# Performance work log

Hardware: AMD Instinct MI355X
Metric: run time of the kernel (lower is better)

The kernel has to match this reference:

```python
import jax, jax.numpy as jnp
import numpy as np
import math

B, S, D, H, DFF = 4, 1024, 1024, 16, 4096
DK = D // H
EPS = 1e-5


def setup_inputs() -> dict:
    key = jax.random.key(0)
    ks = jax.random.split(key, 16)
    sc = 0.02
    inp = {
        "x": jax.random.normal(ks[0], (B, S, D), jnp.float32),
        "Wq": jax.random.normal(ks[1], (D, D), jnp.float32) * sc,
        "bq": jnp.zeros((D,), jnp.float32),
        "Wk": jax.random.normal(ks[2], (D, D), jnp.float32) * sc,
        "bk": jnp.zeros((D,), jnp.float32),
        "Wv": jax.random.normal(ks[3], (D, D), jnp.float32) * sc,
        "bv": jnp.zeros((D,), jnp.float32),
        "Wo": jax.random.normal(ks[4], (D, D), jnp.float32) * sc,
        "bo": jnp.zeros((D,), jnp.float32),
        "W1": jax.random.normal(ks[5], (D, DFF), jnp.float32) * sc,
        "b1": jnp.zeros((DFF,), jnp.float32),
        "W2": jax.random.normal(ks[6], (DFF, D), jnp.float32) * sc,
        "b2": jnp.zeros((D,), jnp.float32),
        "g1": jnp.ones((D,), jnp.float32),
        "be1": jnp.zeros((D,), jnp.float32),
        "g2": jnp.ones((D,), jnp.float32),
        "be2": jnp.zeros((D,), jnp.float32),
    }
    return inp


def _layernorm(x, g, b):
    mu = jnp.mean(x, axis=-1, keepdims=True)
    var = jnp.mean(jnp.square(x - mu), axis=-1, keepdims=True)
    return (x - mu) * jax.lax.rsqrt(var + EPS) * g + b


def reference(x, Wq, bq, Wk, bk, Wv, bv, Wo, bo, W1, b1, W2, b2, g1, be1, g2, be2):
    # multi-head self-attention (dropout = identity, eval mode)
    q = (x @ Wq + bq).reshape(B, S, H, DK).transpose(0, 2, 1, 3)  # [B,H,S,DK]
    k = (x @ Wk + bk).reshape(B, S, H, DK).transpose(0, 2, 1, 3)
    v = (x @ Wv + bv).reshape(B, S, H, DK).transpose(0, 2, 1, 3)
    scores = jnp.einsum("bhqd,bhkd->bhqk", q, k) / math.sqrt(DK)
    attn_weights = jax.nn.softmax(scores, axis=-1)
    ctx = jnp.einsum("bhqk,bhkd->bhqd", attn_weights, v)
    ctx = ctx.transpose(0, 2, 1, 3).reshape(B, S, D)
    attn_out = ctx @ Wo + bo
    x = _layernorm(x + attn_out, g1, be1)
    ff = jax.nn.relu(x @ W1 + b1) @ W2 + b2
    x = _layernorm(x + ff, g2, be2)
    return x, attn_weights
```

## Files before the change

### kernel.cpp

```cpp
#include <hip/hip_runtime.h>

typedef unsigned short u16;
typedef __attribute__((ext_vector_type(8))) short bf16x8;
typedef __attribute__((ext_vector_type(8))) unsigned short u16x8;
typedef __attribute__((ext_vector_type(4))) float f32x4;

__device__ __forceinline__ u16 f2b(float f) {
  unsigned u = __float_as_uint(f);
  u += 0x7fffu + ((u >> 16) & 1u);
  return (u16)(u >> 16);
}

__global__ __launch_bounds__(256) void cast_k(const float* __restrict__ s,
                                              u16* __restrict__ d, int n4) {
  int i = blockIdx.x * 256 + threadIdx.x;
  if (i >= n4) return;
  float4 v = *(const float4*)(s + (size_t)i * 4);
  ushort4 o = make_ushort4(f2b(v.x), f2b(v.y), f2b(v.z), f2b(v.w));
  *(ushort4*)(d + (size_t)i * 4) = o;
}

__global__ __launch_bounds__(256) void transpose_k(const float* __restrict__ src,
                                                   u16* __restrict__ dst,
                                                   int ldsrc, int lddst) {
  __shared__ float t[32][33];
  int c0 = blockIdx.x * 32, r0 = blockIdx.y * 32;
  int tx = threadIdx.x, ty = threadIdx.y;
#pragma unroll
  for (int i = 0; i < 4; ++i)
    t[ty + i * 8][tx] = src[(size_t)(r0 + ty + i * 8) * ldsrc + c0 + tx];
  __syncthreads();
#pragma unroll
  for (int i = 0; i < 4; ++i)
    dst[(size_t)(c0 + ty + i * 8) * lddst + r0 + tx] = f2b(t[tx][ty + i * 8]);
}

__global__ __launch_bounds__(256) void transpose_v_k(const u16* __restrict__ qkv,
                                                     u16* __restrict__ vt) {
  __shared__ u16 t[32][33];
  int z = blockIdx.z;
  int b = z >> 4, h = z & 15;
  int s0 = blockIdx.x * 32, d0 = blockIdx.y * 32;
  int tx = threadIdx.x, ty = threadIdx.y;
  const u16* src = qkv + (size_t)(b * 1024) * 3072 + 2048 + h * 64;
  u16* dst = vt + (size_t)z * 65536;
#pragma unroll
  for (int i = 0; i < 4; ++i)
    t[ty + i * 8][tx] = src[(size_t)(s0 + ty + i * 8) * 3072 + d0 + tx];
  __syncthreads();
#pragma unroll
  for (int i = 0; i < 4; ++i)
    dst[(size_t)(d0 + ty + i * 8) * 1024 + s0 + tx] = t[tx][ty + i * 8];
}

template <int BN, int AF32, int BIAS, int RELU, int SB16, int SF32>
__global__ __launch_bounds__(256) void gemm_k(
    const u16* __restrict__ Ab, const float* __restrict__ Af,
    long aHi, long aLo, int lda,
    const u16* __restrict__ Bt, long bHi, long bLo, int ldb,
    float* __restrict__ Cf, u16* __restrict__ Cb,
    long cHi, long cLo, int ldc,
    const float* __restrict__ bias, int K, int ZD) {
  constexpr int NT = BN / 32;
  __shared__ u16 As[128 * 40];
  __shared__ u16 Bs[BN * 40];

  const int tid = threadIdx.x;
  const int lane = tid & 63;
  const int wave = tid >> 6;
  const int waveM = wave >> 1, waveN = wave & 1;
  const int quad = lane >> 4, l16 = lane & 15;

  const int zb = blockIdx.z / ZD, zr = blockIdx.z % ZD;
  const long aOff = zb * aHi + zr * aLo;
  const long bOff = zb * bHi + zr * bLo;
  const long cOff = zb * cHi + zr * cLo;

  const int row0 = blockIdx.y * 128;
  const int col0 = blockIdx.x * BN;

  f32x4 acc[4][NT] = {};

  for (int k0 = 0; k0 < K; k0 += 32) {
#pragma unroll
    for (int it = 0; it < 2; ++it) {
      int e = (it * 256 + tid) * 8;
      int r = e >> 5, c = e & 31;
      if (AF32) {
        const float4* p = (const float4*)(Af + aOff + (long)(row0 + r) * lda + k0 + c);
        float4 v0 = p[0], v1 = p[1];
        u16x8 wv;
        wv[0] = f2b(v0.x); wv[1] = f2b(v0.y); wv[2] = f2b(v0.z); wv[3] = f2b(v0.w);
        wv[4] = f2b(v1.x); wv[5] = f2b(v1.y); wv[6] = f2b(v1.z); wv[7] = f2b(v1.w);
        *(u16x8*)&As[r * 40 + c] = wv;
      } else {
        uint4 v = *(const uint4*)(Ab + aOff + (long)(row0 + r) * lda + k0 + c);
        *(uint4*)&As[r * 40 + c] = v;
      }
    }
#pragma unroll
    for (int it = 0; it < BN / 64; ++it) {
      int e = (it * 256 + tid) * 8;
      int r = e >> 5, c = e & 31;
      uint4 v = *(const uint4*)(Bt + bOff + (long)(col0 + r) * ldb + k0 + c);
      *(uint4*)&Bs[r * 40 + c] = v;
    }
    __syncthreads();

    bf16x8 af[4], bfr[NT];
#pragma unroll
    for (int mi = 0; mi < 4; ++mi)
      af[mi] = *(const bf16x8*)&As[(waveM * 64 + mi * 16 + l16) * 40 + quad * 8];
#pragma unroll
    for (int ni = 0; ni < NT; ++ni)
      bfr[ni] = *(const bf16x8*)&Bs[(waveN * (BN / 2) + ni * 16 + l16) * 40 + quad * 8];
#pragma unroll
    for (int mi = 0; mi < 4; ++mi)
#pragma unroll
      for (int ni = 0; ni < NT; ++ni)
        acc[mi][ni] = __builtin_amdgcn_mfma_f32_16x16x32_bf16(af[mi], bfr[ni], acc[mi][ni], 0, 0, 0);
    __syncthreads();
  }

#pragma unroll
  for (int ni = 0; ni < NT; ++ni) {
    int col = col0 + waveN * (BN / 2) + ni * 16 + l16;
    float bv = BIAS ? bias[col] : 0.f;
#pragma unroll
    for (int mi = 0; mi < 4; ++mi) {
#pragma unroll
      for (int r = 0; r < 4; ++r) {
        int row = row0 + waveM * 64 + mi * 16 + quad * 4 + r;
        float v = acc[mi][ni][r] + bv;
        if (RELU) v = fmaxf(v, 0.f);
        long idx = cOff + (long)row * ldc + col;
        if (SF32) Cf[idx] = v;
        if (SB16) Cb[idx] = f2b(v);
      }
    }
  }
}

__global__ __launch_bounds__(256) void softmax_k(float* __restrict__ a) {
  long row = blockIdx.x;
  int tid = threadIdx.x;
  float* p = a + row * 1024 + tid * 4;
  float4 v = *(const float4*)p;
  float m = fmaxf(fmaxf(v.x, v.y), fmaxf(v.z, v.w));
#pragma unroll
  for (int d = 32; d > 0; d >>= 1) m = fmaxf(m, __shfl_xor(m, d));
  __shared__ float red[4];
  if ((tid & 63) == 0) red[tid >> 6] = m;
  __syncthreads();
  m = fmaxf(fmaxf(red[0], red[1]), fmaxf(red[2], red[3]));
  v.x = __expf((v.x - m) * 0.125f);
  v.y = __expf((v.y - m) * 0.125f);
  v.z = __expf((v.z - m) * 0.125f);
  v.w = __expf((v.w - m) * 0.125f);
  float s = v.x + v.y + v.z + v.w;
#pragma unroll
  for (int d = 32; d > 0; d >>= 1) s += __shfl_xor(s, d);
  __shared__ float red2[4];
  if ((tid & 63) == 0) red2[tid >> 6] = s;
  __syncthreads();
  s = red2[0] + red2[1] + red2[2] + red2[3];
  float r = 1.f / s;
  v.x *= r; v.y *= r; v.z *= r; v.w *= r;
  *(float4*)p = v;
}

template <int WB16>
__global__ __launch_bounds__(256) void add_ln_k(const float* __restrict__ xp,
                                                const float* __restrict__ yp,
                                                const float* __restrict__ g,
                                                const float* __restrict__ bta,
                                                float* __restrict__ of,
                                                u16* __restrict__ ob) {
  long row = blockIdx.x;
  int tid = threadIdx.x;
  const float4 xv = *(const float4*)(xp + row * 1024 + tid * 4);
  const float4 yv = *(const float4*)(yp + row * 1024 + tid * 4);
  float4 v = make_float4(xv.x + yv.x, xv.y + yv.y, xv.z + yv.z, xv.w + yv.w);
  float s1 = v.x + v.y + v.z + v.w;
  float s2 = v.x * v.x + v.y * v.y + v.z * v.z + v.w * v.w;
#pragma unroll
  for (int d = 32; d > 0; d >>= 1) {
    s1 += __shfl_xor(s1, d);
    s2 += __shfl_xor(s2, d);
  }
  __shared__ float r1[4], r2[4];
  if ((tid & 63) == 0) { r1[tid >> 6] = s1; r2[tid >> 6] = s2; }
  __syncthreads();
  s1 = r1[0] + r1[1] + r1[2] + r1[3];
  s2 = r2[0] + r2[1] + r2[2] + r2[3];
  float mu = s1 * (1.f / 1024.f);
  float var = s2 * (1.f / 1024.f) - mu * mu;
  float rs = rsqrtf(var + 1e-5f);
  float4 gv = *(const float4*)(g + tid * 4);
  float4 bv = *(const float4*)(bta + tid * 4);
  float4 o;
  o.x = (v.x - mu) * rs * gv.x + bv.x;
  o.y = (v.y - mu) * rs * gv.y + bv.y;
  o.z = (v.z - mu) * rs * gv.z + bv.z;
  o.w = (v.w - mu) * rs * gv.w + bv.w;
  *(float4*)(of + row * 1024 + tid * 4) = o;
  if (WB16) {
    ushort4 ov = make_ushort4(f2b(o.x), f2b(o.y), f2b(o.z), f2b(o.w));
    *(ushort4*)(ob + row * 1024 + tid * 4) = ov;
  }
}

extern "C" void kernel_launch(void* const* d_in, const int* in_sizes, int n_in,
                              void* d_out, int out_size, void* d_ws, size_t ws_size,
                              hipStream_t stream) {
  const float* x   = (const float*)d_in[0];
  const float* Wq  = (const float*)d_in[1];
  const float* bq  = (const float*)d_in[2];
  const float* Wk  = (const float*)d_in[3];
  const float* bk  = (const float*)d_in[4];
  const float* Wv  = (const float*)d_in[5];
  const float* bv  = (const float*)d_in[6];
  const float* Wo  = (const float*)d_in[7];
  const float* bo  = (const float*)d_in[8];
  const float* W1  = (const float*)d_in[9];
  const float* b1  = (const float*)d_in[10];
  const float* W2  = (const float*)d_in[11];
  const float* b2  = (const float*)d_in[12];
  const float* g1  = (const float*)d_in[13];
  const float* be1 = (const float*)d_in[14];
  const float* g2  = (const float*)d_in[15];
  const float* be2 = (const float*)d_in[16];

  float* out = (float*)d_out;
  float* attn = out + 4194304LL;

  char* w = (char*)d_ws;
  size_t off = 0;
  auto alloc = [&](size_t bytes) {
    void* p = w + off;
    off = (off + bytes + 255) & ~(size_t)255;
    return p;
  };
  u16* xb        = (u16*)alloc(8388608);
  u16* Wqkvt     = (u16*)alloc(6291456);
  u16* Wot       = (u16*)alloc(2097152);
  u16* W1t       = (u16*)alloc(8388608);
  u16* W2t       = (u16*)alloc(8388608);
  float* bqkv    = (float*)alloc(12288);
  u16* qkvb      = (u16*)alloc(25165824);
  u16* vtb       = (u16*)alloc(8388608);
  u16* ctxb      = (u16*)alloc(8388608);
  float* attn_o  = (float*)alloc(16777216);
  float* x1      = (float*)alloc(16777216);
  u16* x1b       = (u16*)alloc(8388608);
  u16* ff1b      = (u16*)alloc(33554432);
  float* ff2     = (float*)alloc(16777216);
  (void)ws_size; (void)in_sizes; (void)n_in; (void)out_size;

  dim3 tb(32, 8);
  cast_k<<<4096, 256, 0, stream>>>(x, xb, 1048576);
  transpose_k<<<dim3(32, 32), tb, 0, stream>>>(Wq, Wqkvt,           1024, 1024);
  transpose_k<<<dim3(32, 32), tb, 0, stream>>>(Wk, Wqkvt + 1048576, 1024, 1024);
  transpose_k<<<dim3(32, 32), tb, 0, stream>>>(Wv, Wqkvt + 2097152, 1024, 1024);
  transpose_k<<<dim3(32, 32), tb, 0, stream>>>(Wo, Wot, 1024, 1024);
  transpose_k<<<dim3(128, 32), tb, 0, stream>>>(W1, W1t, 4096, 1024);
  transpose_k<<<dim3(32, 128), tb, 0, stream>>>(W2, W2t, 1024, 4096);
  hipMemcpyAsync(bqkv,        bq, 4096, hipMemcpyDeviceToDevice, stream);
  hipMemcpyAsync(bqkv + 1024, bk, 4096, hipMemcpyDeviceToDevice, stream);
  hipMemcpyAsync(bqkv + 2048, bv, 4096, hipMemcpyDeviceToDevice, stream);

  gemm_k<128, 0, 1, 0, 1, 0><<<dim3(24, 32, 1), 256, 0, stream>>>(
      xb, nullptr, 0, 0, 1024, Wqkvt, 0, 0, 1024,
      nullptr, qkvb, 0, 0, 3072, bqkv, 1024, 1);

  transpose_v_k<<<dim3(32, 2, 64), tb, 0, stream>>>(qkvb, vtb);

  gemm_k<128, 0, 0, 0, 0, 1><<<dim3(8, 8, 64), 256, 0, stream>>>(
      qkvb, nullptr, 3145728, 64, 3072,
      qkvb + 1024, 3145728, 64, 3072,
      attn, nullptr, 16777216, 1048576, 1024, nullptr, 64, 16);

  softmax_k<<<65536, 256, 0, stream>>>(attn);

  gemm_k<64, 1, 0, 0, 1, 0><<<dim3(1, 8, 64), 256, 0, stream>>>(
      nullptr, attn, 16777216, 1048576, 1024,
      vtb, 1048576, 65536, 1024,
      nullptr, ctxb, 1048576, 64, 1024, nullptr, 1024, 16);

  gemm_k<128, 0, 1, 0, 0, 1><<<dim3(8, 32, 1), 256, 0, stream>>>(
      ctxb, nullptr, 0, 0, 1024, Wot, 0, 0, 1024,
      attn_o, nullptr, 0, 0, 1024, bo, 1024, 1);

  add_ln_k<1><<<4096, 256, 0, stream>>>(x, attn_o, g1, be1, x1, x1b);

  gemm_k<128, 0, 1, 1, 1, 0><<<dim3(32, 32, 1), 256, 0, stream>>>(
      x1b, nullptr, 0, 0, 1024, W1t, 0, 0, 1024,
      nullptr, ff1b, 0, 0, 4096, b1, 1024, 1);

  gemm_k<128, 0, 1, 0, 0, 1><<<dim3(8, 32, 1), 256, 0, stream>>>(
      ff1b, nullptr, 0, 0, 4096, W2t, 0, 0, 4096,
      ff2, nullptr, 0, 0, 1024, b2, 4096, 1);

  add_ln_k<0><<<4096, 256, 0, stream>>>(x1, ff2, g2, be2, out, nullptr);
}
```

Measured before the change: 822.8 us.

## Fuse softmax into PV GEMM and use direct global-to-LDS loads

```diff
diff --git a/kernel.cpp b/kernel.cpp
--- a/kernel.cpp
+++ b/kernel.cpp
@@ -2,13 +2,18 @@
 
 typedef unsigned short u16;
 typedef __attribute__((ext_vector_type(8))) short bf16x8;
-typedef __attribute__((ext_vector_type(8))) unsigned short u16x8;
 typedef __attribute__((ext_vector_type(4))) float f32x4;
 
 __device__ __forceinline__ u16 f2b(float f) {
   unsigned u = __float_as_uint(f);
   u += 0x7fffu + ((u >> 16) & 1u);
   return (u16)(u >> 16);
+}
+
+__device__ __forceinline__ void load_lds16(const void* g, void* l) {
+  __builtin_amdgcn_global_load_lds(
+      (const __attribute__((address_space(1))) unsigned int*)g,
+      (__attribute__((address_space(3))) unsigned int*)l, 16, 0, 0);
 }
 
 __global__ __launch_bounds__(256) void cast_k(const float* __restrict__ s,
@@ -53,23 +58,24 @@
     dst[(size_t)(d0 + ty + i * 8) * 1024 + s0 + tx] = t[tx][ty + i * 8];
 }
 
-template <int BN, int AF32, int BIAS, int RELU, int SB16, int SF32>
+template <int BN, int BIAS, int RELU, int SB16, int SF32>
 __global__ __launch_bounds__(256) void gemm_k(
-    const u16* __restrict__ Ab, const float* __restrict__ Af,
-    long aHi, long aLo, int lda,
+    const u16* __restrict__ A, long aHi, long aLo, int lda,
     const u16* __restrict__ Bt, long bHi, long bLo, int ldb,
     float* __restrict__ Cf, u16* __restrict__ Cb,
     long cHi, long cLo, int ldc,
     const float* __restrict__ bias, int K, int ZD) {
   constexpr int NT = BN / 32;
-  __shared__ u16 As[128 * 40];
-  __shared__ u16 Bs[BN * 40];
+  __shared__ u16 As[128 * 32];
+  __shared__ u16 Bs[BN * 32];
 
   const int tid = threadIdx.x;
   const int lane = tid & 63;
   const int wave = tid >> 6;
   const int waveM = wave >> 1, waveN = wave & 1;
   const int quad = lane >> 4, l16 = lane & 15;
+  const int lr = lane >> 2;
+  const int lc = (lane & 3) * 8;
 
   const int zb = blockIdx.z / ZD, zr = blockIdx.z % ZD;
   const long aOff = zb * aHi + zr * aLo;
@@ -84,36 +90,25 @@
   for (int k0 = 0; k0 < K; k0 += 32) {
 #pragma unroll
     for (int it = 0; it < 2; ++it) {
-      int e = (it * 256 + tid) * 8;
-      int r = e >> 5, c = e & 31;
-      if (AF32) {
-        const float4* p = (const float4*)(Af + aOff + (long)(row0 + r) * lda + k0 + c);
-        float4 v0 = p[0], v1 = p[1];
-        u16x8 wv;
-        wv[0] = f2b(v0.x); wv[1] = f2b(v0.y); wv[2] = f2b(v0.z); wv[3] = f2b(v0.w);
-        wv[4] = f2b(v1.x); wv[5] = f2b(v1.y); wv[6] = f2b(v1.z); wv[7] = f2b(v1.w);
-        *(u16x8*)&As[r * 40 + c] = wv;
-      } else {
-        uint4 v = *(const uint4*)(Ab + aOff + (long)(row0 + r) * lda + k0 + c);
-        *(uint4*)&As[r * 40 + c] = v;
-      }
+      int rbase = it * 64 + wave * 16;
+      load_lds16(A + aOff + (long)(row0 + rbase + lr) * lda + k0 + lc,
+                 &As[rbase * 32]);
     }
 #pragma unroll
     for (int it = 0; it < BN / 64; ++it) {
-      int e = (it * 256 + tid) * 8;
-      int r = e >> 5, c = e & 31;
-      uint4 v = *(const uint4*)(Bt + bOff + (long)(col0 + r) * ldb + k0 + c);
-      *(uint4*)&Bs[r * 40 + c] = v;
+      int rbase = it * 64 + wave * 16;
+      load_lds16(Bt + bOff + (long)(col0 + rbase + lr) * ldb + k0 + lc,
+                 &Bs[rbase * 32]);
     }
     __syncthreads();
 
     bf16x8 af[4], bfr[NT];
 #pragma unroll
     for (int mi = 0; mi < 4; ++mi)
-      af[mi] = *(const bf16x8*)&As[(waveM * 64 + mi * 16 + l16) * 40 + quad * 8];
+      af[mi] = *(const bf16x8*)&As[(waveM * 64 + mi * 16 + l16) * 32 + quad * 8];
 #pragma unroll
     for (int ni = 0; ni < NT; ++ni)
-      bfr[ni] = *(const bf16x8*)&Bs[(waveN * (BN / 2) + ni * 16 + l16) * 40 + quad * 8];
+      bfr[ni] = *(const bf16x8*)&Bs[(waveN * (BN / 2) + ni * 16 + l16) * 32 + quad * 8];
 #pragma unroll
     for (int mi = 0; mi < 4; ++mi)
 #pragma unroll
@@ -141,32 +136,92 @@
   }
 }
 
-__global__ __launch_bounds__(256) void softmax_k(float* __restrict__ a) {
-  long row = blockIdx.x;
-  int tid = threadIdx.x;
-  float* p = a + row * 1024 + tid * 4;
-  float4 v = *(const float4*)p;
-  float m = fmaxf(fmaxf(v.x, v.y), fmaxf(v.z, v.w));
-#pragma unroll
-  for (int d = 32; d > 0; d >>= 1) m = fmaxf(m, __shfl_xor(m, d));
-  __shared__ float red[4];
-  if ((tid & 63) == 0) red[tid >> 6] = m;
+__global__ __launch_bounds__(256) void attn_pv_k(float* __restrict__ attn,
+                                                 const u16* __restrict__ vt,
+                                                 u16* __restrict__ ctx) {
+  __shared__ u16 As[128 * 32];
+  __shared__ u16 Bs[64 * 32];
+  __shared__ float rinv[128];
+
+  const int tid = threadIdx.x;
+  const int lane = tid & 63;
+  const int wave = tid >> 6;
+  const int waveM = wave >> 1, waveN = wave & 1;
+  const int quad = lane >> 4, l16 = lane & 15;
+  const int lr = lane >> 2, lc = (lane & 3) * 8;
+
+  const int bh = blockIdx.y;
+  const int b = bh >> 4, h = bh & 15;
+  float* S = attn + (size_t)bh * 1048576 + (size_t)blockIdx.x * 131072;
+  const u16* V = vt + (size_t)bh * 65536;
+  u16* C = ctx + (size_t)b * 1048576 + h * 64 + (size_t)blockIdx.x * 131072;
+
+  for (int i = 0; i < 32; ++i) {
+    int r = wave * 32 + i;
+    const float4* p = (const float4*)(S + (size_t)r * 1024) + lane;
+    float s = 0.f;
+#pragma unroll
+    for (int j = 0; j < 4; ++j) {
+      float4 v = p[j * 64];
+      s += __expf(v.x * 0.125f) + __expf(v.y * 0.125f) +
+           __expf(v.z * 0.125f) + __expf(v.w * 0.125f);
+    }
+#pragma unroll
+    for (int d = 32; d > 0; d >>= 1) s += __shfl_xor(s, d);
+    if (lane == 0) rinv[r] = 1.f / s;
+  }
   __syncthreads();
-  m = fmaxf(fmaxf(red[0], red[1]), fmaxf(red[2], red[3]));
-  v.x = __expf((v.x - m) * 0.125f);
-  v.y = __expf((v.y - m) * 0.125f);
-  v.z = __expf((v.z - m) * 0.125f);
-  v.w = __expf((v.w - m) * 0.125f);
-  float s = v.x + v.y + v.z + v.w;
-#pragma unroll
-  for (int d = 32; d > 0; d >>= 1) s += __shfl_xor(s, d);
-  __shared__ float red2[4];
-  if ((tid & 63) == 0) red2[tid >> 6] = s;
-  __syncthreads();
-  s = red2[0] + red2[1] + red2[2] + red2[3];
-  float r = 1.f / s;
-  v.x *= r; v.y *= r; v.z *= r; v.w *= r;
-  *(float4*)p = v;
+
+  f32x4 acc[4][2] = {};
+  const int srow = tid >> 3;
+  const int scol = (tid & 7) * 4;
+
+  for (int k0 = 0; k0 < 1024; k0 += 32) {
+    load_lds16(V + (long)(wave * 16 + lr) * 1024 + k0 + lc, &Bs[wave * 16 * 32]);
+#pragma unroll
+    for (int pass = 0; pass < 4; ++pass) {
+      int r = pass * 32 + srow;
+      float* p = S + (size_t)r * 1024 + k0 + scol;
+      float4 v = *(const float4*)p;
+      float ri = rinv[r];
+      float4 o;
+      o.x = __expf(v.x * 0.125f) * ri;
+      o.y = __expf(v.y * 0.125f) * ri;
+      o.z = __expf(v.z * 0.125f) * ri;
+      o.w = __expf(v.w * 0.125f) * ri;
+      *(float4*)p = o;
+      ushort4 h4 = make_ushort4(f2b(o.x), f2b(o.y), f2b(o.z), f2b(o.w));
+      *(ushort4*)&As[r * 32 + scol] = h4;
+    }
+    __syncthreads();
+
+    bf16x8 af[4], bfr[2];
+#pragma unroll
+    for (int mi = 0; mi < 4; ++mi)
+      af[mi] = *(const bf16x8*)&As[(waveM * 64 + mi * 16 + l16) * 32 + quad * 8];
+#pragma unroll
+    for (int ni = 0; ni < 2; ++ni)
+      bfr[ni] = *(const bf16x8*)&Bs[(waveN * 32 + ni * 16 + l16) * 32 + quad * 8];
+#pragma unroll
+    for (int mi = 0; mi < 4; ++mi)
+#pragma unroll
+      for (int ni = 0; ni < 2; ++ni)
+        acc[mi][ni] = __builtin_amdgcn_mfma_f32_16x16x32_bf16(af[mi], bfr[ni], acc[mi][ni], 0, 0, 0);
+    __syncthreads();
+  }
+
+#pragma unroll
+  for (int ni = 0; ni < 2; ++ni) {
+    int col = waveN * 32 + ni * 16 + l16;
+#pragma unroll
+    for (int mi = 0; mi < 4; ++mi) {
+#pragma unroll
+      for (int r = 0; r < 4; ++r) {
+        int row = waveM * 64 + mi * 16 + quad * 4 + r;
+        C[(size_t)row * 1024 + col] = f2b(acc[mi][ni][r]);
+      }
+    }
+  }
 }
 
 template <int WB16>
@@ -269,36 +324,31 @@
   hipMemcpyAsync(bqkv + 1024, bk, 4096, hipMemcpyDeviceToDevice, stream);
   hipMemcpyAsync(bqkv + 2048, bv, 4096, hipMemcpyDeviceToDevice, stream);
 
-  gemm_k<128, 0, 1, 0, 1, 0><<<dim3(24, 32, 1), 256, 0, stream>>>(
-      xb, nullptr, 0, 0, 1024, Wqkvt, 0, 0, 1024,
+  gemm_k<128, 1, 0, 1, 0><<<dim3(24, 32, 1), 256, 0, stream>>>(
+      xb, 0, 0, 1024, Wqkvt, 0, 0, 1024,
       nullptr, qkvb, 0, 0, 3072, bqkv, 1024, 1);
 
   transpose_v_k<<<dim3(32, 2, 64), tb, 0, stream>>>(qkvb, vtb);
 
-  gemm_k<128, 0, 0, 0, 0, 1><<<dim3(8, 8, 64), 256, 0, stream>>>(
-      qkvb, nullptr, 3145728, 64, 3072,
+  gemm_k<128, 0, 0, 0, 1><<<dim3(8, 8, 64), 256, 0, stream>>>(
+      qkvb, 3145728, 64, 3072,
       qkvb + 1024, 3145728, 64, 3072,
       attn, nullptr, 16777216, 1048576, 1024, nullptr, 64, 16);
 
-  softmax_k<<<65536, 256, 0, stream>>>(attn);
-
-  gemm_k<64, 1, 0, 0, 1, 0><<<dim3(1, 8, 64), 256, 0, stream>>>(
-      nullptr, attn, 16777216, 1048576, 1024,
-      vtb, 1048576, 65536, 1024,
-      nullptr, ctxb, 1048576, 64, 1024, nullptr, 1024, 16);
-
-  gemm_k<128, 0, 1, 0, 0, 1><<<dim3(8, 32, 1), 256, 0, stream>>>(
-      ctxb, nullptr, 0, 0, 1024, Wot, 0, 0, 1024,
+  attn_pv_k<<<dim3(8, 64), 256, 0, stream>>>(attn, vtb, ctxb);
+
+  gemm_k<128, 1, 0, 0, 1><<<dim3(8, 32, 1), 256, 0, stream>>>(
+      ctxb, 0, 0, 1024, Wot, 0, 0, 1024,
       attn_o, nullptr, 0, 0, 1024, bo, 1024, 1);
 
   add_ln_k<1><<<4096, 256, 0, stream>>>(x, attn_o, g1, be1, x1, x1b);
 
-  gemm_k<128, 0, 1, 1, 1, 0><<<dim3(32, 32, 1), 256, 0, stream>>>(
-      x1b, nullptr, 0, 0, 1024, W1t, 0, 0, 1024,
+  gemm_k<128, 1, 1, 1, 0><<<dim3(32, 32, 1), 256, 0, stream>>>(
+      x1b, 0, 0, 1024, W1t, 0, 0, 1024,
       nullptr, ff1b, 0, 0, 4096, b1, 1024, 1);
 
-  gemm_k<128, 0, 1, 0, 0, 1><<<dim3(8, 32, 1), 256, 0, stream>>>(
-      ff1b, nullptr, 0, 0, 4096, W2t, 0, 0, 4096,
+  gemm_k<128, 1, 0, 0, 1><<<dim3(8, 32, 1), 256, 0, stream>>>(
+      ff1b, 0, 0, 4096, W2t, 0, 0, 4096,
       ff2, nullptr, 0, 0, 1024, b2, 4096, 1);
 
   add_ln_k<0><<<4096, 256, 0, stream>>>(x1, ff2, g2, be2, out, nullptr);
```

After: 835.6 us. No clear change (+1.6%).
